# Kernel tuning notes

Measured on AMD Instinct MI355X. Metric: run time of the kernel, lower is better.

Reference implementation:

```python
import jax, jax.numpy as jnp
import numpy as np
from jax.scipy.special import logsumexp

GRID_N = 512
N_ITERS = 5


def _build_grid(n):
    nH = n * (n - 1)
    E = 2 * n * (n - 1)
    P = (n - 1) * (n - 1)
    N = n * n
    pi, pj = np.meshgrid(np.arange(n - 1), np.arange(n - 1), indexing='ij')
    pi, pj = pi.ravel(), pj.ravel()
    # child edges of plaquette (i,j): top/bottom horizontal, left/right vertical
    pce = np.stack([pi * (n - 1) + pj,
                    (pi + 1) * (n - 1) + pj,
                    nH + pi * n + pj,
                    nH + pi * n + pj + 1], 1).astype(np.int32)
    epp = np.zeros((E, 2), np.int32)
    eps = np.zeros((E, 2), np.int32)
    epm = np.zeros((E, 2), np.float32)
    ev = np.zeros((E, 2), np.int32)
    hi, hj = np.meshgrid(np.arange(n), np.arange(n - 1), indexing='ij')
    hi, hj = hi.ravel(), hj.ravel()
    he = hi * (n - 1) + hj
    m = hi < n - 1
    epp[he[m], 0] = hi[m] * (n - 1) + hj[m]; epm[he[m], 0] = 1; eps[he, 0] = 0
    m = hi > 0
    epp[he[m], 1] = (hi[m] - 1) * (n - 1) + hj[m]; epm[he[m], 1] = 1; eps[he, 1] = 1
    ev[he, 0] = hi * n + hj; ev[he, 1] = hi * n + hj + 1
    vi, vj = np.meshgrid(np.arange(n - 1), np.arange(n), indexing='ij')
    vi, vj = vi.ravel(), vj.ravel()
    ve = nH + vi * n + vj
    m = vj < n - 1
    epp[ve[m], 0] = vi[m] * (n - 1) + vj[m]; epm[ve[m], 0] = 1; eps[ve, 0] = 2
    m = vj > 0
    epp[ve[m], 1] = vi[m] * (n - 1) + vj[m] - 1; epm[ve[m], 1] = 1; eps[ve, 1] = 3
    ev[ve, 0] = vi * n + vj; ev[ve, 1] = (vi + 1) * n + vj
    return epp, eps, epm, pce, ev, E, P, N


def setup_inputs() -> dict:
    n = GRID_N
    epp, eps, epm, pce, ev, E, P, N = _build_grid(n)
    key = jax.random.key(0)
    k1, k2 = jax.random.split(key)
    return {
        'log_phi_plaq': 0.5 * jax.random.normal(k1, (P, 2, 2, 2, 2), jnp.float32),
        'log_phi_edge': 0.5 * jax.random.normal(k2, (E, 2, 2), jnp.float32),
        'edge_parent_plaq': jnp.asarray(epp),
        'edge_parent_slot': jnp.asarray(eps),
        'edge_parent_mask': jnp.asarray(epm),
        'plaq_child_edge': jnp.asarray(pce),
        'edge_vars': jnp.asarray(ev),
        'n_iters': N_ITERS,
        'n_vars': N,
    }


def _forward(log_phi_plaq, log_phi_edge, epp, eps, epm, pce, ev, n_iters, n_vars):
    P = log_phi_plaq.shape[0]
    maskNN = epm[:, :, None, None]

    def edge_totals(logM):
        # sum of log-messages from (<=2) parents into each edge, plus edge factor
        g = logM[epp, eps]                      # [E,2,2,2]
        return log_phi_edge + jnp.sum(g * maskNN, axis=1)  # [E,2,2]

    def plaq_terms(logM, tot):
        n_all = tot[pce] - logM                 # [P,4,2,2]: child msg excluding this parent
        b0 = n_all[:, 0, :, :, None, None]      # top edge -> vars (a,b)
        b1 = n_all[:, 1, None, None, :, :]      # bottom  -> vars (c,d)
        b2 = n_all[:, 2, :, None, :, None]      # left    -> vars (a,c)
        b3 = n_all[:, 3, None, :, None, :]      # right   -> vars (b,d)
        S = log_phi_plaq + b0 + b1 + b2 + b3    # [P,2,2,2,2] plaquette log-belief (unnorm)
        return S, (b0, b1, b2, b3)

    def step(logM, _):
        tot = edge_totals(logM)
        S, (b0, b1, b2, b3) = plaq_terms(logM, tot)
        m0 = logsumexp(S - b0, axis=(3, 4))
        m1 = logsumexp(S - b1, axis=(1, 2))
        m2 = logsumexp(S - b2, axis=(2, 4))
        m3 = logsumexp(S - b3, axis=(1, 3))
        new = jnp.stack([m0, m1, m2, m3], axis=1)
        new = new - logsumexp(new, axis=(2, 3), keepdims=True)  # normalize messages
        return new, None

    logM0 = jnp.full((P, 4, 2, 2), -jnp.log(4.0), log_phi_plaq.dtype)
    logM, _ = jax.lax.scan(step, logM0, None, length=n_iters)

    tot = edge_totals(logM)
    log_b_e = tot - logsumexp(tot, axis=(1, 2), keepdims=True)
    S, _ = plaq_terms(logM, tot)
    log_b_p = S - logsumexp(S, axis=(1, 2, 3, 4), keepdims=True)
    b_e = jnp.exp(log_b_e)
    b_p = jnp.exp(log_b_p)

    # Kikuchi free energy: c_plaq = 1, c_edge = 1 - #parents
    c_e = 1.0 - jnp.sum(epm, axis=1)
    F = (jnp.sum(b_p * (log_b_p - log_phi_plaq))
         + jnp.sum(c_e * jnp.sum(b_e * (log_b_e - log_phi_edge), axis=(1, 2))))

    binary_marginals = b_e                      # every pair is an R1 region
    pa = b_e.sum(axis=2)                        # [E,2] marginal of first var
    pb = b_e.sum(axis=1)                        # [E,2] marginal of second var
    ones = jnp.ones((ev.shape[0],), b_e.dtype)
    node_sum = (jax.ops.segment_sum(pa, ev[:, 0], num_segments=n_vars)
                + jax.ops.segment_sum(pb, ev[:, 1], num_segments=n_vars))
    deg = (jax.ops.segment_sum(ones, ev[:, 0], num_segments=n_vars)
           + jax.ops.segment_sum(ones, ev[:, 1], num_segments=n_vars))
    unary_marginals = node_sum / deg[:, None]   # [N,2]
    return -F, unary_marginals, binary_marginals


def reference(log_phi_plaq, log_phi_edge, edge_parent_plaq, edge_parent_slot,
              edge_parent_mask, plaq_child_edge, edge_vars, n_iters, n_vars):
    return _forward(log_phi_plaq, log_phi_edge, edge_parent_plaq, edge_parent_slot,
                    edge_parent_mask, plaq_child_edge, edge_vars, n_iters, n_vars)
```

## Files before the change

### kernel.cpp

```cpp
#include <hip/hip_runtime.h>
#include <hip/hip_fp16.h>
#include <math.h>


#define CORE 22
#define REG  32
#define NTHR 1024

static __device__ __forceinline__ float4 ld4(const float* p){ return *(const float4*)p; }
static __device__ __forceinline__ float rcpf(float x){ return __builtin_amdgcn_rcpf(x); }

__global__ __attribute__((amdgpu_waves_per_eu(4,4))) __launch_bounds__(NTHR)
void fused_kernel(const float* __restrict__ phiP, const float* __restrict__ phiE,
                  float* __restrict__ outBin, float* __restrict__ Pblk,
                  int m, int n)
{
  __shared__ __half2 pln[2][8][REG*REG];
  const int r = threadIdx.x;
  const int base_i = (int)blockIdx.y*CORE - 5;
  const int base_j = (int)blockIdx.x*CORE - 5;
  const int nH = n*m;

  const int ry = r >> 5, rx = r & 31;
  const int gi = base_i + ry, gj = base_j + rx;
  const int ci = min(max(gi,0), m-1), cj = min(max(gj,0), m-1);
  const bool m0 = gi > 0, m1 = gi < m-1, m2 = gj > 0, m3 = gj < m-1;
  const int r0 = max(ry-1,0)*REG + rx;
  const int r1 = min(ry+1,REG-1)*REG + rx;
  const int r2 = ry*REG + max(rx-1,0);
  const int r3 = ry*REG + min(rx+1,REG-1);
  const bool core = (ry >= 5) && (ry < 5+CORE) && (gi < m) &&
                    (rx >= 5) && (rx < 5+CORE) && (gj < m);

  float peE[16], phE[16];
  {
    float4 v;
    v = ld4(phiE + 4*(size_t)(ci*m+cj));
    peE[0]=__expf(v.x); peE[1]=__expf(v.y); peE[2]=__expf(v.z); peE[3]=__expf(v.w);
    v = ld4(phiE + 4*(size_t)((ci+1)*m+cj));
    peE[4]=__expf(v.x); peE[5]=__expf(v.y); peE[6]=__expf(v.z); peE[7]=__expf(v.w);
    v = ld4(phiE + 4*(size_t)(nH+ci*n+cj));
    peE[8]=__expf(v.x); peE[9]=__expf(v.y); peE[10]=__expf(v.z); peE[11]=__expf(v.w);
    v = ld4(phiE + 4*(size_t)(nH+ci*n+cj+1));
    peE[12]=__expf(v.x); peE[13]=__expf(v.y); peE[14]=__expf(v.z); peE[15]=__expf(v.w);
    const float* pp = phiP + 16*(size_t)(ci*m+cj);
    #pragma unroll
    for (int h=0; h<4; ++h){
      v = ld4(pp + 4*h);
      phE[4*h+0]=__expf(v.x); phE[4*h+1]=__expf(v.y);
      phE[4*h+2]=__expf(v.z); phE[4*h+3]=__expf(v.w);
    }
  }

  float outp[16];
  for (int it=0; it<5; ++it){
    const int cb = it & 1, nb = cb ^ 1;

    float na[4][4];
    if (it == 0){
      #pragma unroll
      for (int k=0;k<16;k++) na[k>>2][k&3] = peE[k];
    } else {
      __half2 a, b; float4 o;
      const float4 one = make_float4(1.f,1.f,1.f,1.f);
      a = pln[cb][2][r0]; b = pln[cb][3][r0];
      o = m0 ? make_float4(__low2float(a),__high2float(a),__low2float(b),__high2float(b)) : one;
      na[0][0]=peE[0]*o.x; na[0][1]=peE[1]*o.y; na[0][2]=peE[2]*o.z; na[0][3]=peE[3]*o.w;
      a = pln[cb][0][r1]; b = pln[cb][1][r1];
      o = m1 ? make_float4(__low2float(a),__high2float(a),__low2float(b),__high2float(b)) : one;
      na[1][0]=peE[4]*o.x; na[1][1]=peE[5]*o.y; na[1][2]=peE[6]*o.z; na[1][3]=peE[7]*o.w;
      a = pln[cb][6][r2]; b = pln[cb][7][r2];
      o = m2 ? make_float4(__low2float(a),__high2float(a),__low2float(b),__high2float(b)) : one;
      na[2][0]=peE[8]*o.x; na[2][1]=peE[9]*o.y; na[2][2]=peE[10]*o.z; na[2][3]=peE[11]*o.w;
      a = pln[cb][4][r3]; b = pln[cb][5][r3];
      o = m3 ? make_float4(__low2float(a),__high2float(a),__low2float(b),__high2float(b)) : one;
      na[3][0]=peE[12]*o.x; na[3][1]=peE[13]*o.y; na[3][2]=peE[14]*o.z; na[3][3]=peE[15]*o.w;
    }

    float g[4][4];
    #pragma unroll
    for (int s=0;s<4;s++){ g[s][0]=0.f; g[s][1]=0.f; g[s][2]=0.f; g[s][3]=0.f; }
    #pragma unroll
    for (int idx=0; idx<16; ++idx){
      const int a=(idx>>3)&1, b=(idx>>2)&1, c=(idx>>1)&1, d=idx&1;
      const int ab=(a<<1)|b, cd=(c<<1)|d, ac=(a<<1)|c, bd=(b<<1)|d;
      float E = (na[0][ab]*na[1][cd]) * (na[2][ac]*na[3][bd]) * phE[idx];
      g[0][ab]+=E; g[1][cd]+=E; g[2][ac]+=E; g[3][bd]+=E;
    }
    #pragma unroll
    for (int s=0;s<4;s++){
      float l1=na[s][0], l2=l1*na[s][1], l3=l2*na[s][2];
      float q2=na[s][3], q1=q2*na[s][2], q0=q1*na[s][1];
      float o0=g[s][0]*q0, o1=g[s][1]*l1*q1, o2=g[s][2]*l2*q2, o3=g[s][3]*l3;
      float inv = rcpf(fmaxf(fmaxf(o0,o1), fmaxf(o2,o3)));
      outp[(s<<2)|0]=o0*inv; outp[(s<<2)|1]=o1*inv;
      outp[(s<<2)|2]=o2*inv; outp[(s<<2)|3]=o3*inv;
    }

    #pragma unroll
    for (int h=0; h<8; ++h)
      pln[nb][h][r] = __floats2half2_rn(outp[2*h], outp[2*h+1]);
    __syncthreads();
  }

  float contrib = 0.f;
  if (core){
    float o5_0[4], o5_2[4], naE5[4][4];
    {
      __half2 a, b; float4 o;
      const float4 one = make_float4(1.f,1.f,1.f,1.f);
      a = pln[1][2][r0]; b = pln[1][3][r0];
      o = m0 ? make_float4(__low2float(a),__high2float(a),__low2float(b),__high2float(b)) : one;
      o5_0[0]=o.x; o5_0[1]=o.y; o5_0[2]=o.z; o5_0[3]=o.w;
      naE5[0][0]=peE[0]*o.x; naE5[0][1]=peE[1]*o.y; naE5[0][2]=peE[2]*o.z; naE5[0][3]=peE[3]*o.w;
      a = pln[1][0][r1]; b = pln[1][1][r1];
      o = m1 ? make_float4(__low2float(a),__high2float(a),__low2float(b),__high2float(b)) : one;
      naE5[1][0]=peE[4]*o.x; naE5[1][1]=peE[5]*o.y; naE5[1][2]=peE[6]*o.z; naE5[1][3]=peE[7]*o.w;
      a = pln[1][6][r2]; b = pln[1][7][r2];
      o = m2 ? make_float4(__low2float(a),__high2float(a),__low2float(b),__high2float(b)) : one;
      o5_2[0]=o.x; o5_2[1]=o.y; o5_2[2]=o.z; o5_2[3]=o.w;
      naE5[2][0]=peE[8]*o.x; naE5[2][1]=peE[9]*o.y; naE5[2][2]=peE[10]*o.z; naE5[2][3]=peE[11]*o.w;
      a = pln[1][4][r3]; b = pln[1][5][r3];
      o = m3 ? make_float4(__low2float(a),__high2float(a),__low2float(b),__high2float(b)) : one;
      naE5[3][0]=peE[12]*o.x; naE5[3][1]=peE[13]*o.y; naE5[3][2]=peE[14]*o.z; naE5[3][3]=peE[15]*o.w;
    }
    {
      float Ln[4][4];
      #pragma unroll
      for (int s=0;s<4;s++)
        #pragma unroll
        for (int k=0;k<4;k++)
          Ln[s][k] = __logf(fmaxf(naE5[s][k], 1e-30f));
      float Z=0.f, accT=0.f;
      #pragma unroll
      for (int idx=0; idx<16; ++idx){
        const int a=(idx>>3)&1, b=(idx>>2)&1, c=(idx>>1)&1, d=idx&1;
        const int ab=(a<<1)|b, cd=(c<<1)|d, ac=(a<<1)|c, bd=(b<<1)|d;
        float E = (naE5[0][ab]*naE5[1][cd]) * (naE5[2][ac]*naE5[3][bd]) * phE[idx];
        float T = (Ln[0][ab]+Ln[1][cd]) + (Ln[2][ac]+Ln[3][bd]);
        Z += E; accT = fmaf(E, T, accT);
      }
      contrib += accT*rcpf(Z) - __logf(Z);
    }
    {
      float P0=naE5[0][0]*outp[0], P1=naE5[0][1]*outp[1],
            P2=naE5[0][2]*outp[2], P3=naE5[0][3]*outp[3];
      float Zt=P0+P1+P2+P3, izt=rcpf(Zt);
      float* ob = outBin + 4*(size_t)(gi*m+gj);
      ob[0]=P0*izt; ob[1]=P1*izt; ob[2]=P2*izt; ob[3]=P3*izt;
      if (gi>0){
        float q0=__logf(fmaxf(o5_0[0]*outp[0],1e-30f));
        float q1=__logf(fmaxf(o5_0[1]*outp[1],1e-30f));
        float q2=__logf(fmaxf(o5_0[2]*outp[2],1e-30f));
        float q3=__logf(fmaxf(o5_0[3]*outp[3],1e-30f));
        contrib += __logf(Zt) - (P0*q0+P1*q1+P2*q2+P3*q3)*izt;
      }
    }
    {
      float P0=naE5[2][0]*outp[8],  P1=naE5[2][1]*outp[9],
            P2=naE5[2][2]*outp[10], P3=naE5[2][3]*outp[11];
      float Zt=P0+P1+P2+P3, izt=rcpf(Zt);
      float* ob = outBin + 4*(size_t)(nH+gi*n+gj);
      ob[0]=P0*izt; ob[1]=P1*izt; ob[2]=P2*izt; ob[3]=P3*izt;
      if (gj>0){
        float q0=__logf(fmaxf(o5_2[0]*outp[8], 1e-30f));
        float q1=__logf(fmaxf(o5_2[1]*outp[9], 1e-30f));
        float q2=__logf(fmaxf(o5_2[2]*outp[10],1e-30f));
        float q3=__logf(fmaxf(o5_2[3]*outp[11],1e-30f));
        contrib += __logf(Zt) - (P0*q0+P1*q1+P2*q2+P3*q3)*izt;
      }
    }
    if (gi == m-1){
      float P0=naE5[1][0]*outp[4], P1=naE5[1][1]*outp[5],
            P2=naE5[1][2]*outp[6], P3=naE5[1][3]*outp[7];
      float izt=rcpf(P0+P1+P2+P3);
      float* ob = outBin + 4*(size_t)((gi+1)*m+gj);
      ob[0]=P0*izt; ob[1]=P1*izt; ob[2]=P2*izt; ob[3]=P3*izt;
    }
    if (gj == m-1){
      float P0=naE5[3][0]*outp[12], P1=naE5[3][1]*outp[13],
            P2=naE5[3][2]*outp[14], P3=naE5[3][3]*outp[15];
      float izt=rcpf(P0+P1+P2+P3);
      float* ob = outBin + 4*(size_t)(nH+gi*n+gj+1);
      ob[0]=P0*izt; ob[1]=P1*izt; ob[2]=P2*izt; ob[3]=P3*izt;
    }
  }

  __syncthreads();
  float* red = (float*)&pln[0][0][0];
  #pragma unroll
  for (int off=32; off>0; off>>=1) contrib += __shfl_down(contrib, off, 64);
  if ((r & 63) == 0) red[r >> 6] = contrib;
  __syncthreads();
  if (r < 16){
    float v = red[r];
    #pragma unroll
    for (int off=8; off>0; off>>=1) v += __shfl_down(v, off, 16);
    if (r == 0) Pblk[blockIdx.y*gridDim.x + blockIdx.x] = v;
  }
}

__global__ __launch_bounds__(256)
void unary_kernel(const float* __restrict__ bin, float* __restrict__ out,
                  const float* __restrict__ Pblk, int m, int n, int nblk)
{
  if (blockIdx.x == 0 && blockIdx.y == 0){
    __shared__ float red[256];
    int tid = threadIdx.y*64 + threadIdx.x;
    float s = 0.f;
    for (int idx = tid; idx < nblk; idx += 256) s += Pblk[idx];
    red[tid] = s; __syncthreads();
    #pragma unroll
    for (int st=128; st>0; st>>=1){
      if (tid < st) red[tid] += red[tid+st];
      __syncthreads();
    }
    if (tid == 0) out[0] = -red[0];
  }
  int j = blockIdx.x*64 + threadIdx.x;
  int i = blockIdx.y*4  + threadIdx.y;
  if (i >= n || j >= n) return;
  const int nH = n*m;
  float s0=0.f, s1=0.f, deg=0.f;
  if (j < m){ const float* b = bin + 4*(size_t)(i*m+j);        s0 += b[0]+b[1]; s1 += b[2]+b[3]; deg+=1.f; }
  if (j > 0){ const float* b = bin + 4*(size_t)(i*m+j-1);      s0 += b[0]+b[2]; s1 += b[1]+b[3]; deg+=1.f; }
  if (i < m){ const float* b = bin + 4*(size_t)(nH+i*n+j);     s0 += b[0]+b[1]; s1 += b[2]+b[3]; deg+=1.f; }
  if (i > 0){ const float* b = bin + 4*(size_t)(nH+(i-1)*n+j); s0 += b[0]+b[2]; s1 += b[1]+b[3]; deg+=1.f; }
  float inv = 1.f/deg;
  size_t v = (size_t)i*n + j;
  out[1+2*v]   = s0*inv;
  out[1+2*v+1] = s1*inv;
}

extern "C" void kernel_launch(void* const* d_in, const int* in_sizes, int n_in,
                              void* d_out, int out_size, void* d_ws, size_t ws_size,
                              hipStream_t stream)
{
  const float* phiP = (const float*)d_in[0];
  const float* phiE = (const float*)d_in[1];
  int P  = in_sizes[0] / 16;
  int m  = (int)(sqrt((double)P) + 0.5);
  int n  = m + 1;
  int N  = n * n;
  float* out  = (float*)d_out;
  float* Pblk = (float*)d_ws;

  int tiles = (m + CORE - 1) / CORE;
  float* outBin = out + 1 + 2*(size_t)N;
  fused_kernel<<<dim3(tiles, tiles), dim3(NTHR), 0, stream>>>(phiP, phiE, outBin, Pblk, m, n);
  unary_kernel<<<dim3((n+63)/64, (n+3)/4), dim3(64,4), 0, stream>>>(outBin, out, Pblk, m, n, tiles*tiles);
}
```

Measured before the change: 151.6 us.

## Halve threads per block with two cells per thread and half-precision potentials

Each block now uses 512 threads, and each thread processes two cells of the 32x32 region in turn. The exponentiated edge and plaquette potentials are kept in registers as packed half2 and unpacked each iteration. The final-stage outputs are re-read from shared memory instead of kept in registers. The aim is to cut register pressure and block size so that more blocks fit per CU (launch bounds of 2). The cost is more serialized work per thread, extra conversions, and fp16 rounding of the potentials, which may affect accuracy.

```diff
diff --git a/kernel.cpp b/kernel.cpp
--- a/kernel.cpp
+++ b/kernel.cpp
@@ -5,106 +5,143 @@
 
 #define CORE 22
 #define REG  32
-#define NTHR 1024
+#define NTHR 512
+#define QC   2
 
 static __device__ __forceinline__ float4 ld4(const float* p){ return *(const float4*)p; }
 static __device__ __forceinline__ float rcpf(float x){ return __builtin_amdgcn_rcpf(x); }
-
-__global__ __attribute__((amdgpu_waves_per_eu(4,4))) __launch_bounds__(NTHR)
+static __device__ __forceinline__ void up4(const __half2* p, int s, float* d){
+  __half2 a = p[2*s], b = p[2*s+1];
+  d[0]=__low2float(a); d[1]=__high2float(a); d[2]=__low2float(b); d[3]=__high2float(b);
+}
+
+__global__ __launch_bounds__(NTHR, 2)
 void fused_kernel(const float* __restrict__ phiP, const float* __restrict__ phiE,
                   float* __restrict__ outBin, float* __restrict__ Pblk,
                   int m, int n)
 {
   __shared__ __half2 pln[2][8][REG*REG];
-  const int r = threadIdx.x;
+  const int t = threadIdx.x;
   const int base_i = (int)blockIdx.y*CORE - 5;
   const int base_j = (int)blockIdx.x*CORE - 5;
   const int nH = n*m;
 
-  const int ry = r >> 5, rx = r & 31;
-  const int gi = base_i + ry, gj = base_j + rx;
-  const int ci = min(max(gi,0), m-1), cj = min(max(gj,0), m-1);
-  const bool m0 = gi > 0, m1 = gi < m-1, m2 = gj > 0, m3 = gj < m-1;
-  const int r0 = max(ry-1,0)*REG + rx;
-  const int r1 = min(ry+1,REG-1)*REG + rx;
-  const int r2 = ry*REG + max(rx-1,0);
-  const int r3 = ry*REG + min(rx+1,REG-1);
-  const bool core = (ry >= 5) && (ry < 5+CORE) && (gi < m) &&
-                    (rx >= 5) && (rx < 5+CORE) && (gj < m);
-
-  float peE[16], phE[16];
-  {
+  __half2 peH[QC][8], phH[QC][8];
+  #pragma unroll
+  for (int q=0; q<QC; ++q){
+    const int r  = t + q*NTHR;
+    const int ry = r >> 5, rx = r & 31;
+    const int gi = base_i + ry, gj = base_j + rx;
+    const int ci = min(max(gi,0), m-1), cj = min(max(gj,0), m-1);
     float4 v;
     v = ld4(phiE + 4*(size_t)(ci*m+cj));
-    peE[0]=__expf(v.x); peE[1]=__expf(v.y); peE[2]=__expf(v.z); peE[3]=__expf(v.w);
+    peH[q][0]=__floats2half2_rn(__expf(v.x),__expf(v.y));
+    peH[q][1]=__floats2half2_rn(__expf(v.z),__expf(v.w));
     v = ld4(phiE + 4*(size_t)((ci+1)*m+cj));
-    peE[4]=__expf(v.x); peE[5]=__expf(v.y); peE[6]=__expf(v.z); peE[7]=__expf(v.w);
+    peH[q][2]=__floats2half2_rn(__expf(v.x),__expf(v.y));
+    peH[q][3]=__floats2half2_rn(__expf(v.z),__expf(v.w));
     v = ld4(phiE + 4*(size_t)(nH+ci*n+cj));
-    peE[8]=__expf(v.x); peE[9]=__expf(v.y); peE[10]=__expf(v.z); peE[11]=__expf(v.w);
+    peH[q][4]=__floats2half2_rn(__expf(v.x),__expf(v.y));
+    peH[q][5]=__floats2half2_rn(__expf(v.z),__expf(v.w));
     v = ld4(phiE + 4*(size_t)(nH+ci*n+cj+1));
-    peE[12]=__expf(v.x); peE[13]=__expf(v.y); peE[14]=__expf(v.z); peE[15]=__expf(v.w);
+    peH[q][6]=__floats2half2_rn(__expf(v.x),__expf(v.y));
+    peH[q][7]=__floats2half2_rn(__expf(v.z),__expf(v.w));
     const float* pp = phiP + 16*(size_t)(ci*m+cj);
     #pragma unroll
     for (int h=0; h<4; ++h){
       v = ld4(pp + 4*h);
-      phE[4*h+0]=__expf(v.x); phE[4*h+1]=__expf(v.y);
-      phE[4*h+2]=__expf(v.z); phE[4*h+3]=__expf(v.w);
-    }
-  }
-
-  float outp[16];
+      phH[q][2*h+0]=__floats2half2_rn(__expf(v.x),__expf(v.y));
+      phH[q][2*h+1]=__floats2half2_rn(__expf(v.z),__expf(v.w));
+    }
+  }
+
   for (int it=0; it<5; ++it){
     const int cb = it & 1, nb = cb ^ 1;
-
-    float na[4][4];
-    if (it == 0){
-      #pragma unroll
-      for (int k=0;k<16;k++) na[k>>2][k&3] = peE[k];
-    } else {
-      __half2 a, b; float4 o;
-      const float4 one = make_float4(1.f,1.f,1.f,1.f);
-      a = pln[cb][2][r0]; b = pln[cb][3][r0];
-      o = m0 ? make_float4(__low2float(a),__high2float(a),__low2float(b),__high2float(b)) : one;
-      na[0][0]=peE[0]*o.x; na[0][1]=peE[1]*o.y; na[0][2]=peE[2]*o.z; na[0][3]=peE[3]*o.w;
-      a = pln[cb][0][r1]; b = pln[cb][1][r1];
-      o = m1 ? make_float4(__low2float(a),__high2float(a),__low2float(b),__high2float(b)) : one;
-      na[1][0]=peE[4]*o.x; na[1][1]=peE[5]*o.y; na[1][2]=peE[6]*o.z; na[1][3]=peE[7]*o.w;
-      a = pln[cb][6][r2]; b = pln[cb][7][r2];
-      o = m2 ? make_float4(__low2float(a),__high2float(a),__low2float(b),__high2float(b)) : one;
-      na[2][0]=peE[8]*o.x; na[2][1]=peE[9]*o.y; na[2][2]=peE[10]*o.z; na[2][3]=peE[11]*o.w;
-      a = pln[cb][4][r3]; b = pln[cb][5][r3];
-      o = m3 ? make_float4(__low2float(a),__high2float(a),__low2float(b),__high2float(b)) : one;
-      na[3][0]=peE[12]*o.x; na[3][1]=peE[13]*o.y; na[3][2]=peE[14]*o.z; na[3][3]=peE[15]*o.w;
-    }
-
-    float g[4][4];
-    #pragma unroll
-    for (int s=0;s<4;s++){ g[s][0]=0.f; g[s][1]=0.f; g[s][2]=0.f; g[s][3]=0.f; }
-    #pragma unroll
-    for (int idx=0; idx<16; ++idx){
-      const int a=(idx>>3)&1, b=(idx>>2)&1, c=(idx>>1)&1, d=idx&1;
-      const int ab=(a<<1)|b, cd=(c<<1)|d, ac=(a<<1)|c, bd=(b<<1)|d;
-      float E = (na[0][ab]*na[1][cd]) * (na[2][ac]*na[3][bd]) * phE[idx];
-      g[0][ab]+=E; g[1][cd]+=E; g[2][ac]+=E; g[3][bd]+=E;
-    }
-    #pragma unroll
-    for (int s=0;s<4;s++){
-      float l1=na[s][0], l2=l1*na[s][1], l3=l2*na[s][2];
-      float q2=na[s][3], q1=q2*na[s][2], q0=q1*na[s][1];
-      float o0=g[s][0]*q0, o1=g[s][1]*l1*q1, o2=g[s][2]*l2*q2, o3=g[s][3]*l3;
-      float inv = rcpf(fmaxf(fmaxf(o0,o1), fmaxf(o2,o3)));
-      outp[(s<<2)|0]=o0*inv; outp[(s<<2)|1]=o1*inv;
-      outp[(s<<2)|2]=o2*inv; outp[(s<<2)|3]=o3*inv;
-    }
-
-    #pragma unroll
-    for (int h=0; h<8; ++h)
-      pln[nb][h][r] = __floats2half2_rn(outp[2*h], outp[2*h+1]);
+    #pragma unroll
+    for (int q=0; q<QC; ++q){
+      const int r  = t + q*NTHR;
+      const int ry = r >> 5, rx = r & 31;
+      const int gi = base_i + ry, gj = base_j + rx;
+      const bool m0 = gi > 0, m1 = gi < m-1, m2 = gj > 0, m3 = gj < m-1;
+      const int r0 = max(ry-1,0)*REG + rx;
+      const int r1 = min(ry+1,REG-1)*REG + rx;
+      const int r2 = ry*REG + max(rx-1,0);
+      const int r3 = ry*REG + min(rx+1,REG-1);
+
+      float pe[16];
+      up4(peH[q],0,pe+0); up4(peH[q],1,pe+4); up4(peH[q],2,pe+8); up4(peH[q],3,pe+12);
+
+      float na[4][4];
+      if (it == 0){
+        #pragma unroll
+        for (int k=0;k<16;k++) na[k>>2][k&3] = pe[k];
+      } else {
+        __half2 a, b; float4 o;
+        const float4 one = make_float4(1.f,1.f,1.f,1.f);
+        a = pln[cb][2][r0]; b = pln[cb][3][r0];
+        o = m0 ? make_float4(__low2float(a),__high2float(a),__low2float(b),__high2float(b)) : one;
+        na[0][0]=pe[0]*o.x; na[0][1]=pe[1]*o.y; na[0][2]=pe[2]*o.z; na[0][3]=pe[3]*o.w;
+        a = pln[cb][0][r1]; b = pln[cb][1][r1];
+        o = m1 ? make_float4(__low2float(a),__high2float(a),__low2float(b),__high2float(b)) : one;
+        na[1][0]=pe[4]*o.x; na[1][1]=pe[5]*o.y; na[1][2]=pe[6]*o.z; na[1][3]=pe[7]*o.w;
+        a = pln[cb][6][r2]; b = pln[cb][7][r2];
+        o = m2 ? make_float4(__low2float(a),__high2float(a),__low2float(b),__high2float(b)) : one;
+        na[2][0]=pe[8]*o.x; na[2][1]=pe[9]*o.y; na[2][2]=pe[10]*o.z; na[2][3]=pe[11]*o.w;
+        a = pln[cb][4][r3]; b = pln[cb][5][r3];
+        o = m3 ? make_float4(__low2float(a),__high2float(a),__low2float(b),__high2float(b)) : one;
+        na[3][0]=pe[12]*o.x; na[3][1]=pe[13]*o.y; na[3][2]=pe[14]*o.z; na[3][3]=pe[15]*o.w;
+      }
+
+      float ph[16];
+      up4(phH[q],0,ph+0); up4(phH[q],1,ph+4); up4(phH[q],2,ph+8); up4(phH[q],3,ph+12);
+
+      float g[4][4];
+      #pragma unroll
+      for (int s=0;s<4;s++){ g[s][0]=0.f; g[s][1]=0.f; g[s][2]=0.f; g[s][3]=0.f; }
+      #pragma unroll
+      for (int idx=0; idx<16; ++idx){
+        const int a=(idx>>3)&1, b=(idx>>2)&1, c=(idx>>1)&1, d=idx&1;
+        const int ab=(a<<1)|b, cd=(c<<1)|d, ac=(a<<1)|c, bd=(b<<1)|d;
+        float E = (na[0][ab]*na[1][cd]) * (na[2][ac]*na[3][bd]) * ph[idx];
+        g[0][ab]+=E; g[1][cd]+=E; g[2][ac]+=E; g[3][bd]+=E;
+      }
+      #pragma unroll
+      for (int s=0;s<4;s++){
+        float l1=na[s][0], l2=l1*na[s][1], l3=l2*na[s][2];
+        float q2=na[s][3], q1=q2*na[s][2], q0=q1*na[s][1];
+        float o0=g[s][0]*q0, o1=g[s][1]*l1*q1, o2=g[s][2]*l2*q2, o3=g[s][3]*l3;
+        float inv = rcpf(fmaxf(fmaxf(o0,o1), fmaxf(o2,o3)));
+        pln[nb][2*s+0][r] = __floats2half2_rn(o0*inv, o1*inv);
+        pln[nb][2*s+1][r] = __floats2half2_rn(o2*inv, o3*inv);
+      }
+    }
     __syncthreads();
   }
 
   float contrib = 0.f;
-  if (core){
+  #pragma unroll
+  for (int q=0; q<QC; ++q){
+    const int r  = t + q*NTHR;
+    const int ry = r >> 5, rx = r & 31;
+    const int gi = base_i + ry, gj = base_j + rx;
+    const bool core = (ry >= 5) && (ry < 5+CORE) && (gi < m) &&
+                      (rx >= 5) && (rx < 5+CORE) && (gj < m);
+    if (!core) continue;
+    const bool m0 = gi > 0, m1 = gi < m-1, m2 = gj > 0, m3 = gj < m-1;
+    const int r0 = max(ry-1,0)*REG + rx;
+    const int r1 = min(ry+1,REG-1)*REG + rx;
+    const int r2 = ry*REG + max(rx-1,0);
+    const int r3 = ry*REG + min(rx+1,REG-1);
+
+    float pe[16], ph[16], own[16];
+    up4(peH[q],0,pe+0); up4(peH[q],1,pe+4); up4(peH[q],2,pe+8); up4(peH[q],3,pe+12);
+    up4(phH[q],0,ph+0); up4(phH[q],1,ph+4); up4(phH[q],2,ph+8); up4(phH[q],3,ph+12);
+    #pragma unroll
+    for (int h=0; h<8; ++h){
+      __half2 a = pln[1][h][r];
+      own[2*h]=__low2float(a); own[2*h+1]=__high2float(a);
+    }
+
     float o5_0[4], o5_2[4], naE5[4][4];
     {
       __half2 a, b; float4 o;
@@ -112,17 +149,17 @@
       a = pln[1][2][r0]; b = pln[1][3][r0];
       o = m0 ? make_float4(__low2float(a),__high2float(a),__low2float(b),__high2float(b)) : one;
       o5_0[0]=o.x; o5_0[1]=o.y; o5_0[2]=o.z; o5_0[3]=o.w;
-      naE5[0][0]=peE[0]*o.x; naE5[0][1]=peE[1]*o.y; naE5[0][2]=peE[2]*o.z; naE5[0][3]=peE[3]*o.w;
+      naE5[0][0]=pe[0]*o.x; naE5[0][1]=pe[1]*o.y; naE5[0][2]=pe[2]*o.z; naE5[0][3]=pe[3]*o.w;
       a = pln[1][0][r1]; b = pln[1][1][r1];
       o = m1 ? make_float4(__low2float(a),__high2float(a),__low2float(b),__high2float(b)) : one;
-      naE5[1][0]=peE[4]*o.x; naE5[1][1]=peE[5]*o.y; naE5[1][2]=peE[6]*o.z; naE5[1][3]=peE[7]*o.w;
+      naE5[1][0]=pe[4]*o.x; naE5[1][1]=pe[5]*o.y; naE5[1][2]=pe[6]*o.z; naE5[1][3]=pe[7]*o.w;
       a = pln[1][6][r2]; b = pln[1][7][r2];
       o = m2 ? make_float4(__low2float(a),__high2float(a),__low2float(b),__high2float(b)) : one;
       o5_2[0]=o.x; o5_2[1]=o.y; o5_2[2]=o.z; o5_2[3]=o.w;
-      naE5[2][0]=peE[8]*o.x; naE5[2][1]=peE[9]*o.y; naE5[2][2]=peE[10]*o.z; naE5[2][3]=peE[11]*o.w;
+      naE5[2][0]=pe[8]*o.x; naE5[2][1]=pe[9]*o.y; naE5[2][2]=pe[10]*o.z; naE5[2][3]=pe[11]*o.w;
       a = pln[1][4][r3]; b = pln[1][5][r3];
       o = m3 ? make_float4(__low2float(a),__high2float(a),__low2float(b),__high2float(b)) : one;
-      naE5[3][0]=peE[12]*o.x; naE5[3][1]=peE[13]*o.y; naE5[3][2]=peE[14]*o.z; naE5[3][3]=peE[15]*o.w;
+      naE5[3][0]=pe[12]*o.x; naE5[3][1]=pe[13]*o.y; naE5[3][2]=pe[14]*o.z; naE5[3][3]=pe[15]*o.w;
     }
     {
       float Ln[4][4];
@@ -136,50 +173,50 @@
       for (int idx=0; idx<16; ++idx){
         const int a=(idx>>3)&1, b=(idx>>2)&1, c=(idx>>1)&1, d=idx&1;
         const int ab=(a<<1)|b, cd=(c<<1)|d, ac=(a<<1)|c, bd=(b<<1)|d;
-        float E = (naE5[0][ab]*naE5[1][cd]) * (naE5[2][ac]*naE5[3][bd]) * phE[idx];
+        float E = (naE5[0][ab]*naE5[1][cd]) * (naE5[2][ac]*naE5[3][bd]) * ph[idx];
         float T = (Ln[0][ab]+Ln[1][cd]) + (Ln[2][ac]+Ln[3][bd]);
         Z += E; accT = fmaf(E, T, accT);
       }
       contrib += accT*rcpf(Z) - __logf(Z);
     }
     {
-      float P0=naE5[0][0]*outp[0], P1=naE5[0][1]*outp[1],
-            P2=naE5[0][2]*outp[2], P3=naE5[0][3]*outp[3];
+      float P0=naE5[0][0]*own[0], P1=naE5[0][1]*own[1],
+            P2=naE5[0][2]*own[2], P3=naE5[0][3]*own[3];
       float Zt=P0+P1+P2+P3, izt=rcpf(Zt);
       float* ob = outBin + 4*(size_t)(gi*m+gj);
       ob[0]=P0*izt; ob[1]=P1*izt; ob[2]=P2*izt; ob[3]=P3*izt;
       if (gi>0){
-        float q0=__logf(fmaxf(o5_0[0]*outp[0],1e-30f));
-        float q1=__logf(fmaxf(o5_0[1]*outp[1],1e-30f));
-        float q2=__logf(fmaxf(o5_0[2]*outp[2],1e-30f));
-        float q3=__logf(fmaxf(o5_0[3]*outp[3],1e-30f));
+        float q0=__logf(fmaxf(o5_0[0]*own[0],1e-30f));
+        float q1=__logf(fmaxf(o5_0[1]*own[1],1e-30f));
+        float q2=__logf(fmaxf(o5_0[2]*own[2],1e-30f));
+        float q3=__logf(fmaxf(o5_0[3]*own[3],1e-30f));
         contrib += __logf(Zt) - (P0*q0+P1*q1+P2*q2+P3*q3)*izt;
       }
     }
     {
-      float P0=naE5[2][0]*outp[8],  P1=naE5[2][1]*outp[9],
-            P2=naE5[2][2]*outp[10], P3=naE5[2][3]*outp[11];
+      float P0=naE5[2][0]*own[8],  P1=naE5[2][1]*own[9],
+            P2=naE5[2][2]*own[10], P3=naE5[2][3]*own[11];
       float Zt=P0+P1+P2+P3, izt=rcpf(Zt);
       float* ob = outBin + 4*(size_t)(nH+gi*n+gj);
       ob[0]=P0*izt; ob[1]=P1*izt; ob[2]=P2*izt; ob[3]=P3*izt;
       if (gj>0){
-        float q0=__logf(fmaxf(o5_2[0]*outp[8], 1e-30f));
-        float q1=__logf(fmaxf(o5_2[1]*outp[9], 1e-30f));
-        float q2=__logf(fmaxf(o5_2[2]*outp[10],1e-30f));
-        float q3=__logf(fmaxf(o5_2[3]*outp[11],1e-30f));
+        float q0=__logf(fmaxf(o5_2[0]*own[8], 1e-30f));
+        float q1=__logf(fmaxf(o5_2[1]*own[9], 1e-30f));
+        float q2=__logf(fmaxf(o5_2[2]*own[10],1e-30f));
+        float q3=__logf(fmaxf(o5_2[3]*own[11],1e-30f));
         contrib += __logf(Zt) - (P0*q0+P1*q1+P2*q2+P3*q3)*izt;
       }
     }
     if (gi == m-1){
-      float P0=naE5[1][0]*outp[4], P1=naE5[1][1]*outp[5],
-            P2=naE5[1][2]*outp[6], P3=naE5[1][3]*outp[7];
+      float P0=naE5[1][0]*own[4], P1=naE5[1][1]*own[5],
+            P2=naE5[1][2]*own[6], P3=naE5[1][3]*own[7];
       float izt=rcpf(P0+P1+P2+P3);
       float* ob = outBin + 4*(size_t)((gi+1)*m+gj);
       ob[0]=P0*izt; ob[1]=P1*izt; ob[2]=P2*izt; ob[3]=P3*izt;
     }
     if (gj == m-1){
-      float P0=naE5[3][0]*outp[12], P1=naE5[3][1]*outp[13],
-            P2=naE5[3][2]*outp[14], P3=naE5[3][3]*outp[15];
+      float P0=naE5[3][0]*own[12], P1=naE5[3][1]*own[13],
+            P2=naE5[3][2]*own[14], P3=naE5[3][3]*own[15];
       float izt=rcpf(P0+P1+P2+P3);
       float* ob = outBin + 4*(size_t)(nH+gi*n+gj+1);
       ob[0]=P0*izt; ob[1]=P1*izt; ob[2]=P2*izt; ob[3]=P3*izt;
@@ -190,13 +227,13 @@
   float* red = (float*)&pln[0][0][0];
   #pragma unroll
   for (int off=32; off>0; off>>=1) contrib += __shfl_down(contrib, off, 64);
-  if ((r & 63) == 0) red[r >> 6] = contrib;
+  if ((t & 63) == 0) red[t >> 6] = contrib;
   __syncthreads();
-  if (r < 16){
-    float v = red[r];
-    #pragma unroll
-    for (int off=8; off>0; off>>=1) v += __shfl_down(v, off, 16);
-    if (r == 0) Pblk[blockIdx.y*gridDim.x + blockIdx.x] = v;
+  if (t < 8){
+    float v = red[t];
+    #pragma unroll
+    for (int off=4; off>0; off>>=1) v += __shfl_down(v, off, 8);
+    if (t == 0) Pblk[blockIdx.y*gridDim.x + blockIdx.x] = v;
   }
 }
 
```

Measured after the change: 144.6 us. 1.05x faster.
